# Performance work log

Hardware: AMD Instinct MI355X
Metric: run time of the kernel (lower is better)

Reference implementation:

```python
import jax, jax.numpy as jnp
import numpy as np

B, T, D_IN, D_OUT, N_FILT, MAX_T = 4, 2048, 512, 512, 24, 2048


def _hankel_filters(max_t: int, k: int) -> np.ndarray:
    # Z_{ij} = 2 / ((i+j)^3 - (i+j)), 1-indexed; top-|eig| eigenvectors
    idx = np.arange(1, max_t + 1, dtype=np.float64)
    ij = idx[None, :] + idx[:, None]
    Z = 2.0 / (ij ** 3 - ij)
    w, v = np.linalg.eigh(Z)
    top = np.argsort(-np.abs(w))[:k]
    return v[:, top].astype(np.float32)  # (max_t, k)


def setup_inputs() -> dict:
    key = jax.random.key(0)
    kx, km = jax.random.split(key)
    x = jax.random.normal(kx, (B, T, D_IN), dtype=jnp.float32)
    filters = jnp.asarray(_hankel_filters(MAX_T, N_FILT))  # (MAX_T, N)
    # nn.Linear weight is (d_out, d_in); stacked -> (N, d_out, d_in)
    scale = 1.0 / np.sqrt(D_IN)
    M_weights = jax.random.uniform(km, (N_FILT, D_OUT, D_IN), dtype=jnp.float32,
                                   minval=-scale, maxval=scale)
    return {"x": x, "filters": filters, "M_weights": M_weights}


def reference(x, filters, M_weights):
    Tlen = x.shape[1]
    phi = filters[:Tlen]                       # (T, N)
    phi_e = phi[None, :, :, None]              # (1, T, N, 1)
    weighted = phi_e * x[:, :, None, :]        # (B, T, N, D_in)
    csum = jnp.cumsum(weighted, axis=1)        # causal cumulative projection
    # per-filter rectangular projection: (B,T,N,f) x (N,o,f) -> (B,T,N,o)
    modulated = jnp.einsum('btnf,nof->btno', csum, M_weights)
    return (phi_e * modulated).sum(axis=2)     # (B, T, D_out)
```

## Files before the change

kernel.cpp:

```cpp
#include <hip/hip_runtime.h>
#include <stdint.h>

#define BQ 4
#define TT 2048
#define DF 512
#define DOUT 512
#define NF 24
#define CHF 8

typedef __attribute__((ext_vector_type(8))) short short8;
typedef __attribute__((ext_vector_type(4))) float f32x4;

typedef __attribute__((address_space(3))) uint8_t       lds_u8;
typedef __attribute__((address_space(1))) const uint8_t glb_u8;

__device__ __forceinline__ float bf2f(unsigned short u) {
    union { unsigned int i; float f; } v; v.i = ((unsigned int)u) << 16; return v.f;
}
__device__ __forceinline__ unsigned short f2bf(float f) {
    union { float f; unsigned int i; } v; v.f = f;
    unsigned int r = v.i + 0x7FFFu + ((v.i >> 16) & 1u);
    return (unsigned short)(r >> 16);
}
__device__ __forceinline__ float lo16f(unsigned int u) { return __uint_as_float(u << 16); }
__device__ __forceinline__ float hi16f(unsigned int u) { return __uint_as_float(u & 0xffff0000u); }

__device__ __forceinline__ int plaus16(unsigned int h) {
    unsigned int e = (h >> 7) & 0xffu;
    return (e >= 97u && e <= 141u) || ((h & 0x7fffu) == 0u);
}

__global__ void k_detect(const unsigned int* __restrict__ X, int* __restrict__ flag)
{
    const int lane = threadIdx.x;
    int cnt = 0;
#pragma unroll
    for (int i = 0; i < 4; ++i) {
        unsigned int w = X[lane * 4 + i];
        cnt += (plaus16(w >> 16) && plaus16(w & 0xffffu)) ? 1 : 0;
    }
    for (int off = 32; off > 0; off >>= 1) cnt += __shfl_down(cnt, off);
    if (lane == 0) *flag = (cnt < 180) ? 1 : 0;
}

__global__ __launch_bounds__(256) void k_convert(
    const void* __restrict__ src, unsigned short* __restrict__ dst,
    const int* __restrict__ flag, int n4)
{
    const int isf32 = *flag;
    int i = blockIdx.x * 256 + threadIdx.x;
    const int stride = gridDim.x * 256;
    for (; i < n4; i += stride) {
        ushort4 o;
        if (isf32) {
            float4 v = ((const float4*)src)[i];
            o.x = f2bf(v.x); o.y = f2bf(v.y); o.z = f2bf(v.z); o.w = f2bf(v.w);
        } else {
            o = ((const ushort4*)src)[i];
        }
        ((ushort4*)dst)[i] = o;
    }
}

__global__ __launch_bounds__(256) void k_convf(
    const void* __restrict__ src, float* __restrict__ dst,
    const int* __restrict__ flag, int n)
{
    const int isf32 = *flag;
    int i = blockIdx.x * 256 + threadIdx.x;
    const int stride = gridDim.x * 256;
    for (; i < n; i += stride)
        dst[i] = isf32 ? ((const float*)src)[i]
                       : bf2f(((const unsigned short*)src)[i]);
}

__global__ __launch_bounds__(256, 3) void k_gemm_fast(
    const unsigned short* __restrict__ X,
    const unsigned short* __restrict__ Mw,
    const float* __restrict__ Fw,
    unsigned short* __restrict__ Z,
    float* __restrict__ Cs,
    int r0)
{
    __shared__ unsigned short sAB[128 * 136];
    __shared__ float sPhi[128];
    unsigned short* const sC = sAB;

    const int tid  = threadIdx.x;
    const int lane = tid & 63;
    const int w    = tid >> 6;
    const int wm   = w & 1, wn = w >> 1;
    const int tm   = blockIdx.x;
    const int on0  = blockIdx.y * 128;
    const int n    = blockIdx.z;

    const int rowg0 = r0 + tm * 128;
    if (tid < 128)
        sPhi[tid] = Fw[((rowg0 + tid) & (TT - 1)) * NF + n];

    const unsigned short* Ag = X + (size_t)rowg0 * DF;
    const unsigned short* Bg = Mw + (size_t)n * DOUT * DF + (size_t)on0 * DF;

    auto stage = [&](int kt, int buf) {
        const unsigned short* Ak = Ag + kt * 32;
        const unsigned short* Bk = Bg + kt * 32;
        lds_u8* base = (lds_u8*)sAB + buf * 16384;
#pragma unroll
        for (int i = 0; i < 2; ++i) {
            const int cbase = i * 256 + w * 64;
            const int c = cbase + lane;
            const int r = c >> 2, qs = c & 3;
            const int qg = qs ^ ((r >> 1) & 3);
            __builtin_amdgcn_global_load_lds(
                (const glb_u8*)(Ak + (size_t)r * DF + qg * 8),
                base + cbase * 16, 16, 0, 0);
            __builtin_amdgcn_global_load_lds(
                (const glb_u8*)(Bk + (size_t)r * DF + qg * 8),
                base + 8192 + cbase * 16, 16, 0, 0);
        }
    };

    f32x4 acc[4][4];
#pragma unroll
    for (int i = 0; i < 4; i++)
#pragma unroll
        for (int j = 0; j < 4; j++) acc[i][j] = (f32x4){0.f, 0.f, 0.f, 0.f};

    stage(0, 0);
    __syncthreads();

    const int lr = lane & 15;
    const int q  = lane >> 4;
    const int qsw = (q ^ ((lr >> 1) & 3)) * 8;

    for (int kt = 0; kt < DF / 32; ++kt) {
        const int cur = kt & 1;
        if (kt < DF / 32 - 1) stage(kt + 1, cur ^ 1);

        const unsigned short* sAc = sAB + cur * 8192;
        const unsigned short* sBc = sAc + 4096;
        short8 a[4], b[4];
#pragma unroll
        for (int i = 0; i < 4; i++)
            a[i] = *(const short8*)&sAc[(wm * 64 + i * 16 + lr) * 32 + qsw];
#pragma unroll
        for (int j = 0; j < 4; j++)
            b[j] = *(const short8*)&sBc[(wn * 64 + j * 16 + lr) * 32 + qsw];
#pragma unroll
        for (int i = 0; i < 4; i++)
#pragma unroll
            for (int j = 0; j < 4; j++)
                acc[i][j] = __builtin_amdgcn_mfma_f32_16x16x32_bf16(
                    a[i], b[j], acc[i][j], 0, 0, 0);

        __syncthreads();
    }

    const int rb = (lane >> 4) * 4;
#pragma unroll
    for (int i = 0; i < 4; i++)
#pragma unroll
        for (int j = 0; j < 4; j++)
#pragma unroll
            for (int r = 0; r < 4; r++) {
                int row = wm * 64 + i * 16 + rb + r;
                sC[row * 136 + wn * 64 + j * 16 + (lane & 15)] =
                    f2bf(acc[i][j][r] * sPhi[row]);
            }
    __syncthreads();

#pragma unroll
    for (int it = 0; it < 8; ++it) {
        int row = it * 16 + (tid >> 4);
        int col = (tid & 15) * 8;
        uint4 v = *(const uint4*)&sC[row * 136 + col];
        *(uint4*)&Z[((size_t)(tm * 128 + row) * NF + n) * 512 + on0 + col] = v;
    }

    {
        const int ci  = tid >> 4;
        const int col = (tid & 15) * 8;
        float s0=0.f,s1=0.f,s2=0.f,s3=0.f,s4=0.f,s5=0.f,s6=0.f,s7=0.f;
#pragma unroll
        for (int r = 0; r < CHF; ++r) {
            uint4 v = *(const uint4*)&sC[(ci * CHF + r) * 136 + col];
            s0 += lo16f(v.x); s1 += hi16f(v.x);
            s2 += lo16f(v.y); s3 += hi16f(v.y);
            s4 += lo16f(v.z); s5 += hi16f(v.z);
            s6 += lo16f(v.w); s7 += hi16f(v.w);
        }
        float* cp = &Cs[((size_t)(tm * 16 + ci) * NF + n) * 512 + on0 + col];
        *(float4*)cp       = make_float4(s0, s1, s2, s3);
        *(float4*)(cp + 4) = make_float4(s4, s5, s6, s7);
    }
}

__global__ __launch_bounds__(256, 2) void k_gemm(
    const void* __restrict__ Xv, const void* __restrict__ Mv,
    const void* __restrict__ Fv, const int* __restrict__ flag,
    unsigned short* __restrict__ Z, int r0, int o0, int W)
{
    __shared__ unsigned short sA[128 * 32];
    __shared__ unsigned short sB[128 * 32];
    __shared__ unsigned short sC[128 * 136];
    __shared__ float sPhi[128];

    const int isf32 = *flag;
    const int tid  = threadIdx.x;
    const int lane = tid & 63;
    const int w    = tid >> 6;
    const int wm   = w & 1, wn = w >> 1;
    const int tm   = blockIdx.x;
    const int on0  = o0 + blockIdx.y * 128;
    const int n    = blockIdx.z;

    const int rowg0 = r0 + tm * 128;
    if (tid < 128) {
        int t = (rowg0 + tid) & (TT - 1);
        sPhi[tid] = isf32 ? ((const float*)Fv)[t * NF + n]
                          : bf2f(((const unsigned short*)Fv)[t * NF + n]);
    }

    const unsigned short* Ah = (const unsigned short*)Xv + (size_t)rowg0 * DF;
    const unsigned short* Bh = (const unsigned short*)Mv +
        (size_t)n * DOUT * DF + (size_t)on0 * DF;
    const float* Af = (const float*)Xv + (size_t)rowg0 * DF;
    const float* Bf = (const float*)Mv + (size_t)n * DOUT * DF + (size_t)on0 * DF;

    f32x4 acc[4][4];
#pragma unroll
    for (int i = 0; i < 4; i++)
#pragma unroll
        for (int j = 0; j < 4; j++) acc[i][j] = (f32x4){0.f, 0.f, 0.f, 0.f};

    for (int kt = 0; kt < DF / 32; ++kt) {
        __syncthreads();
        if (!isf32) {
            const unsigned short* Ak = Ah + kt * 32;
            const unsigned short* Bk = Bh + kt * 32;
#pragma unroll
            for (int i = 0; i < 2; ++i) {
                const int c = i * 256 + tid;
                const int r = c >> 2, cc = (c & 3) * 8;
                *(short8*)&sA[r * 32 + cc] = *(const short8*)(Ak + (size_t)r * DF + cc);
                *(short8*)&sB[r * 32 + cc] = *(const short8*)(Bk + (size_t)r * DF + cc);
            }
        } else {
            const float* Ak = Af + kt * 32;
            const float* Bk = Bf + kt * 32;
#pragma unroll
            for (int i = 0; i < 2; ++i) {
                const int c = i * 256 + tid;
                const int r = c >> 2, cc = (c & 3) * 8;
                float4 a0 = *(const float4*)(Ak + (size_t)r * DF + cc);
                float4 a1 = *(const float4*)(Ak + (size_t)r * DF + cc + 4);
                float4 b0 = *(const float4*)(Bk + (size_t)r * DF + cc);
                float4 b1 = *(const float4*)(Bk + (size_t)r * DF + cc + 4);
                short8 sa, sb;
                sa[0]=(short)f2bf(a0.x); sa[1]=(short)f2bf(a0.y);
                sa[2]=(short)f2bf(a0.z); sa[3]=(short)f2bf(a0.w);
                sa[4]=(short)f2bf(a1.x); sa[5]=(short)f2bf(a1.y);
                sa[6]=(short)f2bf(a1.z); sa[7]=(short)f2bf(a1.w);
                sb[0]=(short)f2bf(b0.x); sb[1]=(short)f2bf(b0.y);
                sb[2]=(short)f2bf(b0.z); sb[3]=(short)f2bf(b0.w);
                sb[4]=(short)f2bf(b1.x); sb[5]=(short)f2bf(b1.y);
                sb[6]=(short)f2bf(b1.z); sb[7]=(short)f2bf(b1.w);
                *(short8*)&sA[r * 32 + cc] = sa;
                *(short8*)&sB[r * 32 + cc] = sb;
            }
        }
        __syncthreads();

        const int lr = lane & 15;
        const int lk = (lane >> 4) * 8;
        short8 a[4], b[4];
#pragma unroll
        for (int i = 0; i < 4; i++)
            a[i] = *(const short8*)&sA[(wm * 64 + i * 16 + lr) * 32 + lk];
#pragma unroll
        for (int j = 0; j < 4; j++)
            b[j] = *(const short8*)&sB[(wn * 64 + j * 16 + lr) * 32 + lk];
#pragma unroll
        for (int i = 0; i < 4; i++)
#pragma unroll
            for (int j = 0; j < 4; j++)
                acc[i][j] = __builtin_amdgcn_mfma_f32_16x16x32_bf16(
                    a[i], b[j], acc[i][j], 0, 0, 0);
    }

    const int rb = (lane >> 4) * 4;
#pragma unroll
    for (int i = 0; i < 4; i++)
#pragma unroll
        for (int j = 0; j < 4; j++)
#pragma unroll
            for (int r = 0; r < 4; r++) {
                int row = wm * 64 + i * 16 + rb + r;
                sC[row * 136 + wn * 64 + j * 16 + (lane & 15)] =
                    f2bf(acc[i][j][r] * sPhi[row]);
            }
    __syncthreads();
#pragma unroll
    for (int it = 0; it < 8; ++it) {
        int row = it * 16 + (tid >> 4);
        int col = (tid & 15) * 8;
        uint4 v = *(const uint4*)&sC[row * 136 + col];
        *(uint4*)&Z[((size_t)(tm * 128 + row) * NF + n) * W + (on0 - o0) + col] = v;
    }
}

__global__ __launch_bounds__(256, 2) void k_csum(
    const unsigned short* __restrict__ Z, float* __restrict__ Cs,
    int W, int CHs)
{
    const int c = blockIdx.x, n = blockIdx.y, tid = threadIdx.x;
    const unsigned short* p = Z + ((size_t)(c * CHs) * NF + n) * W + tid * 2;
    float sx = 0.f, sy = 0.f;
#pragma unroll 8
    for (int t = 0; t < CHs; ++t) {
        unsigned int u = *(const unsigned int*)(p + (size_t)t * NF * W);
        sx += lo16f(u);
        sy += hi16f(u);
    }
    float2* q = (float2*)&Cs[((size_t)c * NF + n) * W + tid * 2];
    *q = make_float2(sx, sy);
}

__global__ __launch_bounds__(256, 4) void k_prefix(
    float* __restrict__ Cs, float* __restrict__ Gc,
    int W, int rr, int nch, int nbat)
{
    const int tid = threadIdx.x;
    const int wave = tid >> 6, lane = tid & 63;
    const int col = blockIdx.x * 4 + wave;
    const int colsPerB = NF * (W / 2);
    const int b = col / colsPerB;
    const int rest = col % colsPerB;
    const int n = rest / (W / 2);
    const int opair = rest % (W / 2);
    float* CsB = Cs + (size_t)b * nch * NF * W;
    const int K = (nch + 63) / 64;
    const int c0 = lane * K;

    float carx = 0.f, cary = 0.f;
    if (nbat == 1 && rr != 0) {
        float2 g = *(const float2*)&Gc[(size_t)n * DOUT + opair * 2];
        carx = g.x; cary = g.y;
    }
    float sx = 0.f, sy = 0.f;
    for (int k = 0; k < K; ++k) {
        int c = c0 + k;
        if (c < nch) {
            float2 v = *(const float2*)&CsB[((size_t)c * NF + n) * W + opair * 2];
            sx += v.x; sy += v.y;
        }
    }
    float ix = sx, iy = sy;
    for (int off = 1; off < 64; off <<= 1) {
        float tx = __shfl_up(ix, off);
        float ty = __shfl_up(iy, off);
        if (lane >= off) { ix += tx; iy += ty; }
    }
    float bx = carx + ix - sx;
    float by = cary + iy - sy;
    for (int k = 0; k < K; ++k) {
        int c = c0 + k;
        if (c < nch) {
            float2* p = (float2*)&CsB[((size_t)c * NF + n) * W + opair * 2];
            float2 v = *p;
            *p = make_float2(bx, by);
            bx += v.x; by += v.y;
        }
    }
    if (nbat == 1 && lane == 63)
        *(float2*)&Gc[(size_t)n * DOUT + opair * 2] = make_float2(carx + ix, cary + iy);
}

#define JLIST(F) F(0) F(1) F(2) F(3) F(4) F(5)

__global__ __launch_bounds__(256, 4) void k_scan(
    const unsigned short* __restrict__ Z, const float* __restrict__ Cs,
    const float* __restrict__ Fw, float* __restrict__ Out,
    int r0, int o0, int W, int CHs)
{
    __shared__ float sPhi[32 * NF];
    __shared__ float2 sP[4][8][64];
    const int cg = blockIdx.x, tid = threadIdx.x;
    const int g = tid >> 6, op = tid & 63;
    const int ng0 = g * 6;
    const int opg = blockIdx.y * 64 + op;
    const int t0g = r0 + cg * CHs;
    const int t0 = t0g & (TT - 1);
    for (int i = tid; i < CHs * NF; i += 256)
        sPhi[i] = Fw[(t0 + i / NF) * NF + (i % NF)];
    __syncthreads();

#define DECLG(j) float gx##j, gy##j;
    JLIST(DECLG)
#define INITG(j) { float2 v = *(const float2*)&Cs[((size_t)cg * NF + ng0 + j) * W + opg * 2]; \
                   gx##j = v.x; gy##j = v.y; }
    JLIST(INITG)

    const unsigned short* zp = Z + ((size_t)cg * CHs * NF + ng0) * W + opg * 2;
    float* outb = Out + (size_t)t0g * DOUT + o0 + blockIdx.y * 128 + op * 2;
    for (int tb = 0; tb < CHs; tb += 8) {
#pragma unroll
        for (int tt = 0; tt < 8; ++tt) {
            float ax = 0.f, ay = 0.f;
            const float* php = &sPhi[(tb + tt) * NF + ng0];
#define UPDG(j) { unsigned int u = *(const unsigned int*)(zp + (size_t)j * W); \
                  gx##j += lo16f(u); gy##j += hi16f(u); \
                  float ph = php[j]; ax += ph * gx##j; ay += ph * gy##j; }
            JLIST(UPDG)
            sP[g][tt][op] = make_float2(ax, ay);
            zp += (size_t)NF * W;
        }
        __syncthreads();
#pragma unroll
        for (int k = 0; k < 2; ++k) {
            const int tt = g * 2 + k;
            float2 p0 = sP[0][tt][op], p1 = sP[1][tt][op],
                   p2 = sP[2][tt][op], p3 = sP[3][tt][op];
            *(float2*)(outb + (size_t)(tb + tt) * DOUT) =
                make_float2(p0.x + p1.x + p2.x + p3.x,
                            p0.y + p1.y + p2.y + p3.y);
        }
        __syncthreads();
    }
}

extern "C" void kernel_launch(void* const* d_in, const int* in_sizes, int n_in,
                              void* d_out, int out_size, void* d_ws, size_t ws_size,
                              hipStream_t stream)
{
    const void* X = d_in[0]; const void* Fil = d_in[1]; const void* Mw = d_in[2];
    for (int i = 0; i < n_in && i < 3; ++i) {
        if (in_sizes[i] == BQ * TT * DF)        X   = d_in[i];
        else if (in_sizes[i] == TT * NF)        Fil = d_in[i];
        else if (in_sizes[i] == NF * DOUT * DF) Mw  = d_in[i];
    }
    float* Out = (float*)d_out;

    const size_t offF = 256;
    const size_t nbF  = (size_t)TT * NF * 4;
    const size_t off0 = offF + nbF;
    const size_t nbX  = (size_t)BQ * TT * DF * 2;
    const size_t nbM  = (size_t)NF * DOUT * DF * 2;
    const size_t nbGc = (size_t)NF * DOUT * 4;

    int* flag = (int*)d_ws;
    float* Fw = (float*)((char*)d_ws + offF);

    hipLaunchKernelGGL(k_detect, dim3(1), dim3(64), 0, stream,
                       (const unsigned int*)X, flag);
    hipLaunchKernelGGL(k_convf, dim3(192), dim3(256), 0, stream,
                       Fil, Fw, flag, TT * NF);

    for (int G = BQ; G >= 2; G >>= 1) {
        const size_t zB  = (size_t)G * TT * NF * 512 * 2;
        const size_t csB = (size_t)(G * TT / CHF) * NF * 512 * 4;
        if (off0 + nbX + nbM + zB + csB > ws_size) continue;

        unsigned short* Xbf = (unsigned short*)((char*)d_ws + off0);
        unsigned short* Mbf = (unsigned short*)((char*)Xbf + nbX);
        unsigned short* Z   = (unsigned short*)((char*)Mbf + nbM);
        float* Cs = (float*)((char*)Z + zB);

        hipLaunchKernelGGL(k_convert, dim3(2048), dim3(256), 0, stream,
                           X, Xbf, flag, BQ * TT * DF / 4);
        hipLaunchKernelGGL(k_convert, dim3(3072), dim3(256), 0, stream,
                           Mw, Mbf, flag, NF * DOUT * DF / 4);

        const int nch = TT / CHF;
        for (int b0 = 0; b0 < BQ; b0 += G) {
            hipLaunchKernelGGL(k_gemm_fast, dim3(G * TT / 128, 4, NF), dim3(256),
                               0, stream, Xbf, Mbf, Fw, Z, Cs, b0 * TT);
            hipLaunchKernelGGL(k_prefix, dim3(G * NF * 256 / 4), dim3(256),
                               0, stream, Cs, (float*)nullptr, 512, 0, nch, G);
            hipLaunchKernelGGL(k_scan, dim3(G * nch, 4), dim3(256), 0, stream,
                               Z, Cs, Fw, Out, b0 * TT, 0, 512, CHF);
        }
        return;
    }

    {
        static const int rts[5] = {2048, 1024, 512, 256, 128};
        int RT = 0;
        for (int ri = 0; ri < 5; ++ri) {
            size_t need = off0 + nbX + nbM
                        + (size_t)rts[ri] * NF * 512 * 2
                        + (size_t)(rts[ri] / CHF) * NF * 512 * 4 + nbGc;
            if (need <= ws_size) { RT = rts[ri]; break; }
        }
        if (RT > 0) {
            unsigned short* Xbf = (unsigned short*)((char*)d_ws + off0);
            unsigned short* Mbf = (unsigned short*)((char*)Xbf + nbX);
            unsigned short* Z   = (unsigned short*)((char*)Mbf + nbM);
            float* Cs = (float*)((char*)Z + (size_t)RT * NF * 512 * 2);
            float* Gc = (float*)((char*)Cs + (size_t)(RT / CHF) * NF * 512 * 4);

            hipLaunchKernelGGL(k_convert, dim3(2048), dim3(256), 0, stream,
                               X, Xbf, flag, BQ * TT * DF / 4);
            hipLaunchKernelGGL(k_convert, dim3(3072), dim3(256), 0, stream,
                               Mw, Mbf, flag, NF * DOUT * DF / 4);

            const int nrr = TT / RT, nch = RT / CHF;
            for (int b = 0; b < BQ; ++b) {
                for (int rr = 0; rr < nrr; ++rr) {
                    const int r0 = b * TT + rr * RT;
                    hipLaunchKernelGGL(k_gemm_fast, dim3(RT / 128, 4, NF), dim3(256),
                                       0, stream, Xbf, Mbf, Fw, Z, Cs, r0);
                    hipLaunchKernelGGL(k_prefix, dim3(NF * 256 / 4), dim3(256),
                                       0, stream, Cs, Gc, 512, rr, nch, 1);
                    hipLaunchKernelGGL(k_scan, dim3(nch, 4), dim3(256), 0, stream,
                                       Z, Cs, Fw, Out, r0, 0, 512, CHF);
                }
            }
            return;
        }
    }

    static const int cRT[7] = {2048, 1024, 512, 256, 128, 128, 128};
    static const int cW[7]  = {512, 512, 512, 512, 512, 256, 128};
    int RTs = 128, W = 128;
    for (int ci = 0; ci < 7; ++ci) {
        size_t need = off0 + (size_t)cRT[ci] * NF * cW[ci] * 2
                    + (size_t)(cRT[ci] / 32) * NF * cW[ci] * 4 + nbGc;
        if (need <= ws_size) { RTs = cRT[ci]; W = cW[ci]; break; }
    }
    unsigned short* Z = (unsigned short*)((char*)d_ws + off0);
    float* Cs = (float*)((char*)Z + (size_t)RTs * NF * W * 2);
    float* Gc = (float*)((char*)Cs + (size_t)(RTs / 32) * NF * W * 4);

    const int nrr = TT / RTs, nch = RTs / 32;
    for (int b = 0; b < BQ; ++b) {
        for (int o0 = 0; o0 < DOUT; o0 += W) {
            for (int rr = 0; rr < nrr; ++rr) {
                const int r0 = b * TT + rr * RTs;
                hipLaunchKernelGGL(k_gemm, dim3(RTs / 128, W / 128, NF), dim3(256),
                                   0, stream, X, Mw, Fil, flag, Z, r0, o0, W);
                hipLaunchKernelGGL(k_csum, dim3(nch, NF), dim3(W / 2), 0, stream,
                                   Z, Cs, W, 32);
                hipLaunchKernelGGL(k_prefix, dim3(NF * (W / 2) / 4), dim3(256),
                                   0, stream, Cs, Gc, W, rr, nch, 1);
                hipLaunchKernelGGL(k_scan, dim3(nch, W / 128), dim3(256), 0, stream,
                                   Z, Cs, Fw, Out, r0, o0, W, 32);
            }
        }
    }
}
```

Measured before the change: 385.0 us.

## Serialize prefix scan per column and widen scan kernel to four outputs

The chunk prefix kernel no longer splits each column across a 64-lane wave with a shuffle scan. It now gives each lane its own output-pair column and walks all chunks serially, with software-pipelined loads, so far fewer blocks are launched. The scan kernel now handles four output columns per thread using uint2 and float4 accesses, which halves its grid in the y dimension. This cuts shuffle and index overhead and widens memory accesses. The cost is fewer threads in flight and a long serial dependency chain per lane in the prefix step.

```diff
diff --git a/kernel.cpp b/kernel.cpp
--- a/kernel.cpp
+++ b/kernel.cpp
@@ -330,50 +330,64 @@
     float* __restrict__ Cs, float* __restrict__ Gc,
     int W, int rr, int nch, int nbat)
 {
-    const int tid = threadIdx.x;
-    const int wave = tid >> 6, lane = tid & 63;
-    const int col = blockIdx.x * 4 + wave;
-    const int colsPerB = NF * (W / 2);
-    const int b = col / colsPerB;
-    const int rest = col % colsPerB;
-    const int n = rest / (W / 2);
-    const int opair = rest % (W / 2);
-    float* CsB = Cs + (size_t)b * nch * NF * W;
-    const int K = (nch + 63) / 64;
-    const int c0 = lane * K;
-
-    float carx = 0.f, cary = 0.f;
+    const int tid  = threadIdx.x;
+    const int lane = tid & 63;
+    const int obw  = W >> 7;
+    const int tasks = nbat * NF * obw;
+    const int gw = blockIdx.x * 4 + (tid >> 6);
+    if (gw >= tasks) return;
+    const int perB = NF * obw;
+    const int b    = gw / perB;
+    const int rest = gw % perB;
+    const int n    = rest / obw;
+    const int ob   = rest % obw;
+    const int opair = ob * 64 + lane;
+
+    float* base = Cs + (size_t)b * nch * NF * W + (size_t)n * W + opair * 2;
+    const size_t cstride = (size_t)NF * W;
+
+    float cx = 0.f, cy = 0.f;
     if (nbat == 1 && rr != 0) {
         float2 g = *(const float2*)&Gc[(size_t)n * DOUT + opair * 2];
-        carx = g.x; cary = g.y;
-    }
-    float sx = 0.f, sy = 0.f;
-    for (int k = 0; k < K; ++k) {
-        int c = c0 + k;
-        if (c < nch) {
-            float2 v = *(const float2*)&CsB[((size_t)c * NF + n) * W + opair * 2];
-            sx += v.x; sy += v.y;
-        }
-    }
-    float ix = sx, iy = sy;
-    for (int off = 1; off < 64; off <<= 1) {
-        float tx = __shfl_up(ix, off);
-        float ty = __shfl_up(iy, off);
-        if (lane >= off) { ix += tx; iy += ty; }
-    }
-    float bx = carx + ix - sx;
-    float by = cary + iy - sy;
-    for (int k = 0; k < K; ++k) {
-        int c = c0 + k;
-        if (c < nch) {
-            float2* p = (float2*)&CsB[((size_t)c * NF + n) * W + opair * 2];
-            float2 v = *p;
-            *p = make_float2(bx, by);
-            bx += v.x; by += v.y;
-        }
-    }
-    if (nbat == 1 && lane == 63)
-        *(float2*)&Gc[(size_t)n * DOUT + opair * 2] = make_float2(carx + ix, cary + iy);
+        cx = g.x; cy = g.y;
+    }
+
+    int c = 0;
+    if (nch >= 16) {
+        float2 v[8], w2[8];
+#pragma unroll
+        for (int k = 0; k < 8; ++k) v[k] = *(float2*)(base + (size_t)k * cstride);
+        for (; c + 16 <= nch; c += 8) {
+#pragma unroll
+            for (int k = 0; k < 8; ++k)
+                w2[k] = *(float2*)(base + (size_t)(c + 8 + k) * cstride);
+#pragma unroll
+            for (int k = 0; k < 8; ++k) {
+                float2* p = (float2*)(base + (size_t)(c + k) * cstride);
+                float2 t = v[k];
+                *p = make_float2(cx, cy);
+                cx += t.x; cy += t.y;
+                v[k] = w2[k];
+            }
+        }
+#pragma unroll
+        for (int k = 0; k < 8; ++k) {
+            float2* p = (float2*)(base + (size_t)(c + k) * cstride);
+            float2 t = v[k];
+            *p = make_float2(cx, cy);
+            cx += t.x; cy += t.y;
+        }
+        c += 8;
+    }
+    for (; c < nch; ++c) {
+        float2* p = (float2*)(base + (size_t)c * cstride);
+        float2 t = *p;
+        *p = make_float2(cx, cy);
+        cx += t.x; cy += t.y;
+    }
+
+    if (nbat == 1)
+        *(float2*)&Gc[(size_t)n * DOUT + opair * 2] = make_float2(cx, cy);
 }
 
 #define JLIST(F) F(0) F(1) F(2) F(3) F(4) F(5)
@@ -384,46 +398,54 @@
     int r0, int o0, int W, int CHs)
 {
     __shared__ float sPhi[32 * NF];
-    __shared__ float2 sP[4][8][64];
+    __shared__ float4 sP[4][8][64];
     const int cg = blockIdx.x, tid = threadIdx.x;
     const int g = tid >> 6, op = tid & 63;
     const int ng0 = g * 6;
-    const int opg = blockIdx.y * 64 + op;
+    const int c4  = (blockIdx.y * 64 + op) * 4;
+    const int act = (c4 + 4 <= W);
+    const int c4u = act ? c4 : (W - 4);
     const int t0g = r0 + cg * CHs;
     const int t0 = t0g & (TT - 1);
     for (int i = tid; i < CHs * NF; i += 256)
         sPhi[i] = Fw[(t0 + i / NF) * NF + (i % NF)];
     __syncthreads();
 
-#define DECLG(j) float gx##j, gy##j;
+#define DECLG(j) float gA##j, gB##j, gC##j, gD##j;
     JLIST(DECLG)
-#define INITG(j) { float2 v = *(const float2*)&Cs[((size_t)cg * NF + ng0 + j) * W + opg * 2]; \
-                   gx##j = v.x; gy##j = v.y; }
+#define INITG(j) { float4 v = *(const float4*)&Cs[((size_t)cg * NF + ng0 + j) * W + c4u]; \
+                   gA##j = v.x; gB##j = v.y; gC##j = v.z; gD##j = v.w; }
     JLIST(INITG)
 
-    const unsigned short* zp = Z + ((size_t)cg * CHs * NF + ng0) * W + opg * 2;
-    float* outb = Out + (size_t)t0g * DOUT + o0 + blockIdx.y * 128 + op * 2;
+    const unsigned short* zp = Z + ((size_t)cg * CHs * NF + ng0) * W + c4u;
+    float* outb = Out + (size_t)t0g * DOUT + o0 + c4;
     for (int tb = 0; tb < CHs; tb += 8) {
 #pragma unroll
         for (int tt = 0; tt < 8; ++tt) {
-            float ax = 0.f, ay = 0.f;
+            float a0 = 0.f, a1 = 0.f, a2 = 0.f, a3 = 0.f;
             const float* php = &sPhi[(tb + tt) * NF + ng0];
-#define UPDG(j) { unsigned int u = *(const unsigned int*)(zp + (size_t)j * W); \
-                  gx##j += lo16f(u); gy##j += hi16f(u); \
-                  float ph = php[j]; ax += ph * gx##j; ay += ph * gy##j; }
+#define UPDG(j) { uint2 u = *(const uint2*)(zp + (size_t)j * W); \
+                  gA##j += lo16f(u.x); gB##j += hi16f(u.x); \
+                  gC##j += lo16f(u.y); gD##j += hi16f(u.y); \
+                  float ph = php[j]; \
+                  a0 += ph * gA##j; a1 += ph * gB##j; \
+                  a2 += ph * gC##j; a3 += ph * gD##j; }
             JLIST(UPDG)
-            sP[g][tt][op] = make_float2(ax, ay);
+            sP[g][tt][op] = make_float4(a0, a1, a2, a3);
             zp += (size_t)NF * W;
         }
         __syncthreads();
 #pragma unroll
         for (int k = 0; k < 2; ++k) {
             const int tt = g * 2 + k;
-            float2 p0 = sP[0][tt][op], p1 = sP[1][tt][op],
+            float4 p0 = sP[0][tt][op], p1 = sP[1][tt][op],
                    p2 = sP[2][tt][op], p3 = sP[3][tt][op];
-            *(float2*)(outb + (size_t)(tb + tt) * DOUT) =
-                make_float2(p0.x + p1.x + p2.x + p3.x,
-                            p0.y + p1.y + p2.y + p3.y);
+            if (act)
+                *(float4*)(outb + (size_t)(tb + tt) * DOUT) =
+                    make_float4(p0.x + p1.x + p2.x + p3.x,
+                                p0.y + p1.y + p2.y + p3.y,
+                                p0.z + p1.z + p2.z + p3.z,
+                                p0.w + p1.w + p2.w + p3.w);
         }
         __syncthreads();
     }
@@ -475,9 +497,9 @@
         for (int b0 = 0; b0 < BQ; b0 += G) {
             hipLaunchKernelGGL(k_gemm_fast, dim3(G * TT / 128, 4, NF), dim3(256),
                                0, stream, Xbf, Mbf, Fw, Z, Cs, b0 * TT);
-            hipLaunchKernelGGL(k_prefix, dim3(G * NF * 256 / 4), dim3(256),
+            hipLaunchKernelGGL(k_prefix, dim3((G * NF * 4 + 3) / 4), dim3(256),
                                0, stream, Cs, (float*)nullptr, 512, 0, nch, G);
-            hipLaunchKernelGGL(k_scan, dim3(G * nch, 4), dim3(256), 0, stream,
+            hipLaunchKernelGGL(k_scan, dim3(G * nch, 2), dim3(256), 0, stream,
                                Z, Cs, Fw, Out, b0 * TT, 0, 512, CHF);
         }
         return;
@@ -510,9 +532,9 @@
                     const int r0 = b * TT + rr * RT;
                     hipLaunchKernelGGL(k_gemm_fast, dim3(RT / 128, 4, NF), dim3(256),
                                        0, stream, Xbf, Mbf, Fw, Z, Cs, r0);
-                    hipLaunchKernelGGL(k_prefix, dim3(NF * 256 / 4), dim3(256),
+                    hipLaunchKernelGGL(k_prefix, dim3((NF * 4 + 3) / 4), dim3(256),
                                        0, stream, Cs, Gc, 512, rr, nch, 1);
-                    hipLaunchKernelGGL(k_scan, dim3(nch, 4), dim3(256), 0, stream,
+                    hipLaunchKernelGGL(k_scan, dim3(nch, 2), dim3(256), 0, stream,
                                        Z, Cs, Fw, Out, r0, 0, 512, CHF);
                 }
             }
@@ -541,11 +563,11 @@
                                    0, stream, X, Mw, Fil, flag, Z, r0, o0, W);
                 hipLaunchKernelGGL(k_csum, dim3(nch, NF), dim3(W / 2), 0, stream,
                                    Z, Cs, W, 32);
-                hipLaunchKernelGGL(k_prefix, dim3(NF * (W / 2) / 4), dim3(256),
+                hipLaunchKernelGGL(k_prefix, dim3((NF * (W / 128) + 3) / 4), dim3(256),
                                    0, stream, Cs, Gc, W, rr, nch, 1);
-                hipLaunchKernelGGL(k_scan, dim3(nch, W / 128), dim3(256), 0, stream,
-                                   Z, Cs, Fw, Out, r0, o0, W, 32);
-            }
-        }
-    }
-}
+                hipLaunchKernelGGL(k_scan, dim3(nch, (W + 255) / 256), dim3(256),
+                                   0, stream, Z, Cs, Fw, Out, r0, o0, W, 32);
+            }
+        }
+    }
+}
```

Measured after the change: 329.5 us. -14.4%, faster.
